# Kernel optimization log

Measured on AMD Instinct MI355X. Metric: run time of the kernel, lower is better.

## Reference

```python
import jax, jax.numpy as jnp
import numpy as np
import math

DIM = 2048
B, Q_LEN, KV_LEN = 8, 128, 4096


def setup_inputs() -> dict:
    key = jax.random.key(0)
    ks = jax.random.split(key, 8)
    x = jax.random.normal(ks[0], (B, Q_LEN, DIM), dtype=jnp.float32)
    mask = jnp.zeros((B, Q_LEN, KV_LEN + Q_LEN), dtype=bool)  # unused by the original forward
    k_cache = jax.random.normal(ks[1], (B, KV_LEN, DIM), dtype=jnp.float32)
    v_cache = jax.random.normal(ks[2], (B, KV_LEN, DIM), dtype=jnp.float32)
    scale = 1.0 / math.sqrt(DIM)
    wq = jax.random.normal(ks[3], (DIM, DIM), dtype=jnp.float32) * scale
    wk = jax.random.normal(ks[4], (DIM, DIM), dtype=jnp.float32) * scale
    wv = jax.random.normal(ks[5], (DIM, DIM), dtype=jnp.float32) * scale
    wo = jax.random.normal(ks[6], (DIM, DIM), dtype=jnp.float32) * scale
    return {"x": x, "mask": mask, "k_cache": k_cache, "v_cache": v_cache,
            "wq": wq, "wk": wk, "wv": wv, "wo": wo}


def reference(x, mask, k_cache, v_cache, wq, wk, wv, wo):
    # Linear layers (torch: y = x @ W^T)
    q = jnp.einsum('bsd,ed->bse', x, wq)
    k_new = jnp.einsum('bsd,ed->bse', x, wk)
    v_new = jnp.einsum('bsd,ed->bse', x, wv)
    # KV-cache growth via concat (the pattern the kernel replaces)
    k = jnp.concatenate([k_cache, k_new], axis=1)  # [B, KV+Q, D]
    v = jnp.concatenate([v_cache, v_new], axis=1)
    scale = 1.0 / math.sqrt(q.shape[-1])
    scores = jnp.einsum('bqd,bkd->bqk', q, k) * scale  # [B, Q, KV+Q]
    attn = jax.nn.softmax(scores, axis=-1)             # NOTE: mask is unused, as in original
    out = jnp.einsum('bqk,bkd->bqd', attn, v)
    return jnp.einsum('bqd,ed->bqe', out, wo)
```

## Files before the change

### kernel.cpp

```cpp
#include <hip/hip_runtime.h>

typedef __bf16 bf16;
typedef __bf16 bf16x4 __attribute__((ext_vector_type(4)));
typedef __bf16 bf16x8 __attribute__((ext_vector_type(8)));
typedef float f32x4 __attribute__((ext_vector_type(4)));

#define DIM   2048
#define BQ    128
#define KVL   4096
#define KVT   4224
#define SCALE 0.022097086912079608f

__device__ __forceinline__ int swz(int row, int col) {
  return row * 64 + (col ^ ((row & 7) << 3));
}

template<int R>
struct PB {
  bf16x8 v[R / 32];
  __device__ __forceinline__ void load(const bf16* __restrict__ src, int ld, int tid) {
    const int r0 = tid >> 3, c = (tid & 7) * 8;
    #pragma unroll
    for (int j = 0; j < R / 32; ++j)
      v[j] = *reinterpret_cast<const bf16x8*>(src + (size_t)(j * 32 + r0) * ld + c);
  }
  __device__ __forceinline__ void write(bf16* dst, int tid) {
    const int r0 = tid >> 3, c = (tid & 7) * 8;
    #pragma unroll
    for (int j = 0; j < R / 32; ++j)
      *reinterpret_cast<bf16x8*>(dst + swz(j * 32 + r0, c)) = v[j];
  }
};

struct PU64 {
  float4 v[4];
  int r0, c;
  __device__ __forceinline__ void init(int tid) { r0 = tid >> 4; c = (tid & 15) * 4; }
  __device__ __forceinline__ void loadF(const float* __restrict__ src, int ld) {
    #pragma unroll
    for (int j = 0; j < 4; ++j)
      v[j] = *reinterpret_cast<const float4*>(src + (size_t)(j * 16 + r0) * ld + c);
  }
  __device__ __forceinline__ void loadB(const bf16* __restrict__ src, int ld) {
    #pragma unroll
    for (int j = 0; j < 4; ++j) {
      bf16x4 t = *reinterpret_cast<const bf16x4*>(src + (size_t)(j * 16 + r0) * ld + c);
      v[j].x = (float)t[0]; v[j].y = (float)t[1]; v[j].z = (float)t[2]; v[j].w = (float)t[3];
    }
  }
  __device__ __forceinline__ void write(bf16* dst) {
    #pragma unroll
    for (int j = 0; j < 4; ++j) {
      bf16x4 b;
      b[0] = (bf16)v[j].x; b[1] = (bf16)v[j].y; b[2] = (bf16)v[j].z; b[3] = (bf16)v[j].w;
      *reinterpret_cast<bf16x4*>(dst + swz(j * 16 + r0, c)) = b;
    }
  }
};

struct PVT {
  float v[16];
  int vn, vk0;
  __device__ __forceinline__ void init(int tid) { vn = tid & 63; vk0 = (tid >> 6) * 16; }
  __device__ __forceinline__ void loadF(const float* __restrict__ src) {
    #pragma unroll
    for (int i = 0; i < 16; ++i) v[i] = src[(size_t)(vk0 + i) * DIM + vn];
  }
  __device__ __forceinline__ void loadB(const bf16* __restrict__ src) {
    #pragma unroll
    for (int i = 0; i < 16; ++i) v[i] = (float)src[(size_t)(vk0 + i) * DIM + vn];
  }
  __device__ __forceinline__ void write(bf16* dst) {
    #pragma unroll
    for (int j = 0; j < 4; ++j) {
      bf16x4 t;
      #pragma unroll
      for (int i = 0; i < 4; ++i) t[i] = (bf16)v[4 * j + i];
      *reinterpret_cast<bf16x4*>(dst + swz(vn, vk0 + 4 * j)) = t;
    }
  }
};

template<int MF, int NF>
__device__ __forceinline__ void mma_tile(const bf16* As, const bf16* Bs,
                                         f32x4 (&acc)[MF][NF], int l, int wm, int wn) {
  const int ar = l & 15;
  const int ak = (l >> 4) * 8;
  bf16x8 a[MF][2], b[NF][2];
  #pragma unroll
  for (int mi = 0; mi < MF; ++mi)
    #pragma unroll
    for (int kk = 0; kk < 2; ++kk)
      a[mi][kk] = *reinterpret_cast<const bf16x8*>(As + swz(wm + mi * 16 + ar, kk * 32 + ak));
  #pragma unroll
  for (int ni = 0; ni < NF; ++ni)
    #pragma unroll
    for (int kk = 0; kk < 2; ++kk)
      b[ni][kk] = *reinterpret_cast<const bf16x8*>(Bs + swz(wn + ni * 16 + ar, kk * 32 + ak));
  #pragma unroll
  for (int kk = 0; kk < 2; ++kk)
    #pragma unroll
    for (int mi = 0; mi < MF; ++mi)
      #pragma unroll
      for (int ni = 0; ni < NF; ++ni)
        acc[mi][ni] = __builtin_amdgcn_mfma_f32_16x16x32_bf16(
            a[mi][kk], b[ni][kk], acc[mi][ni], 0, 0, 0);
}

__global__ __launch_bounds__(256) void k_cvt(const float* __restrict__ x,
    const float* __restrict__ wq, const float* __restrict__ wk,
    const float* __restrict__ wv, const float* __restrict__ wo,
    bf16* __restrict__ xb, bf16* __restrict__ wb) {
  const int seg = blockIdx.y;
  const float* src; bf16* dst; int n; float sc = 1.0f;
  if (seg == 0)      { src = x;  dst = xb;            n = 1024 * DIM; }
  else if (seg == 1) { src = wq; dst = wb;            n = DIM * DIM; sc = SCALE; }
  else if (seg == 2) { src = wk; dst = wb + 1 * DIM * DIM; n = DIM * DIM; }
  else if (seg == 3) { src = wv; dst = wb + 2 * DIM * DIM; n = DIM * DIM; }
  else               { src = wo; dst = wb + 3 * DIM * DIM; n = DIM * DIM; }
  const int i0 = (blockIdx.x * 256 + threadIdx.x) * 8;
  if (i0 >= n) return;
  #pragma unroll
  for (int h = 0; h < 2; ++h) {
    float4 v = *reinterpret_cast<const float4*>(src + i0 + 4 * h);
    bf16x4 b;
    b[0] = (bf16)(v.x * sc); b[1] = (bf16)(v.y * sc);
    b[2] = (bf16)(v.z * sc); b[3] = (bf16)(v.w * sc);
    *reinterpret_cast<bf16x4*>(dst + i0 + 4 * h) = b;
  }
}

__global__ __launch_bounds__(256) void k_qkv(const bf16* __restrict__ xb,
    const bf16* __restrict__ wb,
    bf16* __restrict__ qb, bf16* __restrict__ kb, bf16* __restrict__ vb) {
  __shared__ bf16 As[2][128 * 64];
  __shared__ bf16 Bs[2][64 * 64];
  const int nt = blockIdx.x;
  const int w  = nt >> 5;
  const int col0 = (nt & 31) * 64;
  bf16* __restrict__ O = (w == 0) ? qb : (w == 1) ? kb : vb;
  const int m0 = blockIdx.y * 128;
  const int tid = threadIdx.x, l = tid & 63, wid = tid >> 6;
  const int wm = (wid >> 1) * 64, wn = (wid & 1) * 32;
  const bf16* Ap = xb + (size_t)m0 * DIM;
  const bf16* Bp = wb + (size_t)nt * 64 * DIM;
  PB<128> pa; PB<64> pbb;
  f32x4 acc[4][2] = {};
  pa.load(Ap, DIM, tid); pbb.load(Bp, DIM, tid);
  pa.write(As[0], tid);  pbb.write(Bs[0], tid);
  int cur = 0;
  constexpr int NT = DIM / 64;
  for (int kt = 0; kt < NT; ++kt) {
    if (kt + 1 < NT) { pa.load(Ap + (kt + 1) * 64, DIM, tid); pbb.load(Bp + (kt + 1) * 64, DIM, tid); }
    __syncthreads();
    mma_tile<4, 2>(As[cur], Bs[cur], acc, l, wm, wn);
    if (kt + 1 < NT) { pa.write(As[cur ^ 1], tid); pbb.write(Bs[cur ^ 1], tid); }
    cur ^= 1;
  }
  const int rr = (l >> 4) * 4, cc = l & 15;
  #pragma unroll
  for (int mi = 0; mi < 4; ++mi)
    #pragma unroll
    for (int ni = 0; ni < 2; ++ni)
      #pragma unroll
      for (int r = 0; r < 4; ++r)
        O[(size_t)(m0 + wm + mi * 16 + rr + r) * DIM + col0 + wn + ni * 16 + cc] =
            (bf16)acc[mi][ni][r];
}

__global__ __launch_bounds__(256) void k_scores(const bf16* __restrict__ qb,
    const bf16* __restrict__ kb, const float* __restrict__ kcache,
    float* __restrict__ scores) {
  __shared__ bf16 As[2][128 * 64];
  __shared__ bf16 Bs[2][64 * 64];
  const int nt = blockIdx.x;
  const int b  = blockIdx.y;
  const int tid = threadIdx.x, l = tid & 63, wid = tid >> 6;
  const int wm = (wid >> 1) * 64, wn = (wid & 1) * 32;
  const bf16* Q = qb + (size_t)b * BQ * DIM;
  const bool useCache = (nt < 64);
  const float* Bf = kcache + ((size_t)b * KVL + nt * 64) * DIM;
  const bf16*  Bb = kb + ((size_t)b * BQ + (nt - 64) * 64) * DIM;
  PB<128> pa; PU64 pu; pu.init(tid);
  f32x4 acc[4][2] = {};
  pa.load(Q, DIM, tid);
  if (useCache) pu.loadF(Bf, DIM); else pu.loadB(Bb, DIM);
  pa.write(As[0], tid); pu.write(Bs[0]);
  int cur = 0;
  constexpr int NT = DIM / 64;
  for (int kt = 0; kt < NT; ++kt) {
    if (kt + 1 < NT) {
      pa.load(Q + (kt + 1) * 64, DIM, tid);
      if (useCache) pu.loadF(Bf + (kt + 1) * 64, DIM); else pu.loadB(Bb + (kt + 1) * 64, DIM);
    }
    __syncthreads();
    mma_tile<4, 2>(As[cur], Bs[cur], acc, l, wm, wn);
    if (kt + 1 < NT) { pa.write(As[cur ^ 1], tid); pu.write(Bs[cur ^ 1]); }
    cur ^= 1;
  }
  const int rr = (l >> 4) * 4, cc = l & 15;
  #pragma unroll
  for (int mi = 0; mi < 4; ++mi)
    #pragma unroll
    for (int ni = 0; ni < 2; ++ni)
      #pragma unroll
      for (int r = 0; r < 4; ++r)
        scores[((size_t)b * BQ + wm + mi * 16 + rr + r) * KVT + nt * 64 + wn + ni * 16 + cc] =
            acc[mi][ni][r];
}

__global__ __launch_bounds__(256) void k_softmax(const float* __restrict__ scores,
                                                 bf16* __restrict__ attn) {
  __shared__ float s[KVT];
  __shared__ float red[8];
  const int row = blockIdx.x;
  const int tid = threadIdx.x;
  const size_t base = (size_t)row * KVT;
  float lm = -1e30f;
  for (int i = tid; i < KVT; i += 256) {
    float v = scores[base + i];
    s[i] = v;
    lm = fmaxf(lm, v);
  }
  #pragma unroll
  for (int off = 32; off >= 1; off >>= 1) lm = fmaxf(lm, __shfl_xor(lm, off, 64));
  if ((tid & 63) == 0) red[tid >> 6] = lm;
  __syncthreads();
  const float m = fmaxf(fmaxf(red[0], red[1]), fmaxf(red[2], red[3]));
  float ls = 0.f;
  for (int i = tid; i < KVT; i += 256) {
    float e = __expf(s[i] - m);
    s[i] = e;
    ls += e;
  }
  #pragma unroll
  for (int off = 32; off >= 1; off >>= 1) ls += __shfl_xor(ls, off, 64);
  if ((tid & 63) == 0) red[4 + (tid >> 6)] = ls;
  __syncthreads();
  const float inv = 1.f / (red[4] + red[5] + red[6] + red[7]);
  for (int i = tid; i < KVT; i += 256) attn[base + i] = (bf16)(s[i] * inv);
}

__global__ __launch_bounds__(256) void k_pv(const bf16* __restrict__ attn,
    const float* __restrict__ vcache, const bf16* __restrict__ vb,
    float* __restrict__ pp) {
  __shared__ bf16 As[2][128 * 64];
  __shared__ bf16 VT[2][64 * 64];
  const int n0 = blockIdx.x * 64;
  const int b  = blockIdx.y;
  const int c  = blockIdx.z;
  const int tid = threadIdx.x, l = tid & 63, wid = tid >> 6;
  const int wm = (wid >> 1) * 64, wn = (wid & 1) * 32;
  const bf16* Ap = attn + (size_t)b * BQ * KVT + c * 2112;
  PB<128> pa; PVT pv; pv.init(tid);
  f32x4 acc[4][2] = {};
  auto loadV = [&](int lk) {
    const int grow = c * 2112 + lk * 64;
    if (grow < KVL) pv.loadF(vcache + ((size_t)b * KVL + grow) * DIM + n0);
    else            pv.loadB(vb + ((size_t)b * BQ + (grow - KVL)) * DIM + n0);
  };
  pa.load(Ap, KVT, tid); loadV(0);
  pa.write(As[0], tid);  pv.write(VT[0]);
  int cur = 0;
  constexpr int NT = 33;
  for (int kt = 0; kt < NT; ++kt) {
    if (kt + 1 < NT) { pa.load(Ap + (kt + 1) * 64, KVT, tid); loadV(kt + 1); }
    __syncthreads();
    mma_tile<4, 2>(As[cur], VT[cur], acc, l, wm, wn);
    if (kt + 1 < NT) { pa.write(As[cur ^ 1], tid); pv.write(VT[cur ^ 1]); }
    cur ^= 1;
  }
  float* P = pp + (size_t)c * 1024 * DIM;
  const int rr = (l >> 4) * 4, cc = l & 15;
  #pragma unroll
  for (int mi = 0; mi < 4; ++mi)
    #pragma unroll
    for (int ni = 0; ni < 2; ++ni)
      #pragma unroll
      for (int r = 0; r < 4; ++r)
        P[((size_t)b * BQ + wm + mi * 16 + rr + r) * DIM + n0 + wn + ni * 16 + cc] =
            acc[mi][ni][r];
}

__global__ __launch_bounds__(256) void k_pvcomb(const float* __restrict__ pp,
                                                bf16* __restrict__ ob) {
  const int i0 = (blockIdx.x * 256 + threadIdx.x) * 4;
  float4 a = *reinterpret_cast<const float4*>(pp + i0);
  float4 b = *reinterpret_cast<const float4*>(pp + 1024 * DIM + i0);
  bf16x4 o;
  o[0] = (bf16)(a.x + b.x); o[1] = (bf16)(a.y + b.y);
  o[2] = (bf16)(a.z + b.z); o[3] = (bf16)(a.w + b.w);
  *reinterpret_cast<bf16x4*>(ob + i0) = o;
}

__global__ __launch_bounds__(256) void k_oproj(const bf16* __restrict__ ob,
    const bf16* __restrict__ wob, float* __restrict__ po) {
  __shared__ bf16 As[2][128 * 64];
  __shared__ bf16 Bs[2][64 * 64];
  const int n0 = blockIdx.x * 64;
  const int m0 = blockIdx.y * 128;
  const int kz = blockIdx.z;
  const int tid = threadIdx.x, l = tid & 63, wid = tid >> 6;
  const int wm = (wid >> 1) * 64, wn = (wid & 1) * 32;
  const bf16* Ap = ob  + (size_t)m0 * DIM + kz * 1024;
  const bf16* Bp = wob + (size_t)n0 * DIM + kz * 1024;
  PB<128> pa; PB<64> pbb;
  f32x4 acc[4][2] = {};
  pa.load(Ap, DIM, tid); pbb.load(Bp, DIM, tid);
  pa.write(As[0], tid);  pbb.write(Bs[0], tid);
  int cur = 0;
  constexpr int NT = 16;
  for (int kt = 0; kt < NT; ++kt) {
    if (kt + 1 < NT) { pa.load(Ap + (kt + 1) * 64, DIM, tid); pbb.load(Bp + (kt + 1) * 64, DIM, tid); }
    __syncthreads();
    mma_tile<4, 2>(As[cur], Bs[cur], acc, l, wm, wn);
    if (kt + 1 < NT) { pa.write(As[cur ^ 1], tid); pbb.write(Bs[cur ^ 1], tid); }
    cur ^= 1;
  }
  float* P = po + (size_t)kz * 1024 * DIM;
  const int rr = (l >> 4) * 4, cc = l & 15;
  #pragma unroll
  for (int mi = 0; mi < 4; ++mi)
    #pragma unroll
    for (int ni = 0; ni < 2; ++ni)
      #pragma unroll
      for (int r = 0; r < 4; ++r)
        P[(size_t)(m0 + wm + mi * 16 + rr + r) * DIM + n0 + wn + ni * 16 + cc] =
            acc[mi][ni][r];
}

__global__ __launch_bounds__(256) void k_ocomb(const float* __restrict__ po,
                                               float* __restrict__ out) {
  const int i0 = (blockIdx.x * 256 + threadIdx.x) * 4;
  float4 a = *reinterpret_cast<const float4*>(po + i0);
  float4 b = *reinterpret_cast<const float4*>(po + 1024 * DIM + i0);
  float4 o = {a.x + b.x, a.y + b.y, a.z + b.z, a.w + b.w};
  *reinterpret_cast<float4*>(out + i0) = o;
}

extern "C" void kernel_launch(void* const* d_in, const int* in_sizes, int n_in,
                              void* d_out, int out_size, void* d_ws, size_t ws_size,
                              hipStream_t stream) {
  const float* x      = (const float*)d_in[0];
  const float* kcache = (const float*)d_in[2];
  const float* vcache = (const float*)d_in[3];
  const float* wq     = (const float*)d_in[4];
  const float* wk     = (const float*)d_in[5];
  const float* wv     = (const float*)d_in[6];
  const float* wo     = (const float*)d_in[7];
  float* out = (float*)d_out;

  char* ws = (char*)d_ws;
  bf16*  xb     = (bf16*)(ws + 0);
  bf16*  wb     = (bf16*)(ws + 4194304);
  bf16*  qb     = (bf16*)(ws + 37748736);
  bf16*  kb     = (bf16*)(ws + 41943040);
  bf16*  vb     = (bf16*)(ws + 46137344);
  float* scores = (float*)(ws + 50331648);
  bf16*  attnb  = (bf16*)(ws + 67633152);
  bf16*  obuf   = (bf16*)(ws + 76283904);
  float* pp     = scores;
  bf16*  wob    = wb + (size_t)3 * DIM * DIM;

  k_cvt<<<dim3(2048, 5), 256, 0, stream>>>(x, wq, wk, wv, wo, xb, wb);
  k_qkv<<<dim3(96, 8), 256, 0, stream>>>(xb, wb, qb, kb, vb);
  k_scores<<<dim3(66, 8), 256, 0, stream>>>(qb, kb, kcache, scores);
  k_softmax<<<dim3(1024), 256, 0, stream>>>(scores, attnb);
  k_pv<<<dim3(32, 8, 2), 256, 0, stream>>>(attnb, vcache, vb, pp);
  k_pvcomb<<<dim3(2048), 256, 0, stream>>>(pp, obuf);
  k_oproj<<<dim3(32, 8, 2), 256, 0, stream>>>(obuf, wob, pp);
  k_ocomb<<<dim3(2048), 256, 0, stream>>>(pp, out);
}
```

Before: 245.6 us.

## Stage bf16 tiles via direct global-to-LDS loads and drop o-proj split-K

Replaces the register-staged bf16 tile loads with direct global-to-LDS loads (global_load_lds) using an XOR chunk swizzle in the qkv, scores, pv and oproj GEMMs, and moves the barrier to after the MMA. This is meant to cut VGPR pressure and the extra LDS write instructions, and to let copies overlap compute. The oproj split-K over two halves and its combine kernel are removed so the projection writes the output directly. This saves a launch and a float round trip but halves the oproj grid to 256 blocks. It also depends on the swizzle matching the reader's layout.

```diff
diff --git a/kernel.cpp b/kernel.cpp
--- a/kernel.cpp
+++ b/kernel.cpp
@@ -15,22 +15,24 @@
   return row * 64 + (col ^ ((row & 7) << 3));
 }
 
-template<int R>
-struct PB {
-  bf16x8 v[R / 32];
-  __device__ __forceinline__ void load(const bf16* __restrict__ src, int ld, int tid) {
-    const int r0 = tid >> 3, c = (tid & 7) * 8;
-    #pragma unroll
-    for (int j = 0; j < R / 32; ++j)
-      v[j] = *reinterpret_cast<const bf16x8*>(src + (size_t)(j * 32 + r0) * ld + c);
-  }
-  __device__ __forceinline__ void write(bf16* dst, int tid) {
-    const int r0 = tid >> 3, c = (tid & 7) * 8;
-    #pragma unroll
-    for (int j = 0; j < R / 32; ++j)
-      *reinterpret_cast<bf16x8*>(dst + swz(j * 32 + r0, c)) = v[j];
-  }
-};
+__device__ __forceinline__ void gload16(const bf16* g, bf16* l) {
+  __builtin_amdgcn_global_load_lds(
+      (const __attribute__((address_space(1))) void*)g,
+      (__attribute__((address_space(3))) void*)l, 16, 0, 0);
+}
+
+template<int R, int NW>
+__device__ __forceinline__ void gstage(const bf16* __restrict__ src, int ld,
+                                       bf16* dst, int wid, int lane) {
+  constexpr int OPS = R / (8 * NW);
+  const int rsub = lane >> 3;
+  const int schunk = (lane & 7) ^ (rsub & 7);
+  #pragma unroll
+  for (int j = 0; j < OPS; ++j) {
+    const int row0 = wid * (R / NW) + j * 8;
+    gload16(src + (size_t)(row0 + rsub) * ld + schunk * 8, dst + row0 * 64);
+  }
+}
 
 struct PU64 {
   float4 v[4];
@@ -144,18 +146,18 @@
   const int wm = (wid >> 1) * 64, wn = (wid & 1) * 32;
   const bf16* Ap = xb + (size_t)m0 * DIM;
   const bf16* Bp = wb + (size_t)nt * 64 * DIM;
-  PB<128> pa; PB<64> pbb;
   f32x4 acc[4][2] = {};
-  pa.load(Ap, DIM, tid); pbb.load(Bp, DIM, tid);
-  pa.write(As[0], tid);  pbb.write(Bs[0], tid);
-  int cur = 0;
+  gstage<128, 4>(Ap, DIM, As[0], wid, l);
+  gstage<64, 4>(Bp, DIM, Bs[0], wid, l);
+  __syncthreads();
   constexpr int NT = DIM / 64;
   for (int kt = 0; kt < NT; ++kt) {
-    if (kt + 1 < NT) { pa.load(Ap + (kt + 1) * 64, DIM, tid); pbb.load(Bp + (kt + 1) * 64, DIM, tid); }
+    if (kt + 1 < NT) {
+      gstage<128, 4>(Ap + (kt + 1) * 64, DIM, As[(kt + 1) & 1], wid, l);
+      gstage<64, 4>(Bp + (kt + 1) * 64, DIM, Bs[(kt + 1) & 1], wid, l);
+    }
+    mma_tile<4, 2>(As[kt & 1], Bs[kt & 1], acc, l, wm, wn);
     __syncthreads();
-    mma_tile<4, 2>(As[cur], Bs[cur], acc, l, wm, wn);
-    if (kt + 1 < NT) { pa.write(As[cur ^ 1], tid); pbb.write(Bs[cur ^ 1], tid); }
-    cur ^= 1;
   }
   const int rr = (l >> 4) * 4, cc = l & 15;
   #pragma unroll
@@ -181,22 +183,21 @@
   const bool useCache = (nt < 64);
   const float* Bf = kcache + ((size_t)b * KVL + nt * 64) * DIM;
   const bf16*  Bb = kb + ((size_t)b * BQ + (nt - 64) * 64) * DIM;
-  PB<128> pa; PU64 pu; pu.init(tid);
+  PU64 pu; pu.init(tid);
   f32x4 acc[4][2] = {};
-  pa.load(Q, DIM, tid);
+  gstage<128, 4>(Q, DIM, As[0], wid, l);
   if (useCache) pu.loadF(Bf, DIM); else pu.loadB(Bb, DIM);
-  pa.write(As[0], tid); pu.write(Bs[0]);
-  int cur = 0;
+  pu.write(Bs[0]);
+  __syncthreads();
   constexpr int NT = DIM / 64;
   for (int kt = 0; kt < NT; ++kt) {
     if (kt + 1 < NT) {
-      pa.load(Q + (kt + 1) * 64, DIM, tid);
+      gstage<128, 4>(Q + (kt + 1) * 64, DIM, As[(kt + 1) & 1], wid, l);
       if (useCache) pu.loadF(Bf + (kt + 1) * 64, DIM); else pu.loadB(Bb + (kt + 1) * 64, DIM);
     }
+    mma_tile<4, 2>(As[kt & 1], Bs[kt & 1], acc, l, wm, wn);
+    if (kt + 1 < NT) pu.write(Bs[(kt + 1) & 1]);
     __syncthreads();
-    mma_tile<4, 2>(As[cur], Bs[cur], acc, l, wm, wn);
-    if (kt + 1 < NT) { pa.write(As[cur ^ 1], tid); pu.write(Bs[cur ^ 1]); }
-    cur ^= 1;
   }
   const int rr = (l >> 4) * 4, cc = l & 15;
   #pragma unroll
@@ -252,23 +253,25 @@
   const int tid = threadIdx.x, l = tid & 63, wid = tid >> 6;
   const int wm = (wid >> 1) * 64, wn = (wid & 1) * 32;
   const bf16* Ap = attn + (size_t)b * BQ * KVT + c * 2112;
-  PB<128> pa; PVT pv; pv.init(tid);
+  PVT pv; pv.init(tid);
   f32x4 acc[4][2] = {};
   auto loadV = [&](int lk) {
     const int grow = c * 2112 + lk * 64;
     if (grow < KVL) pv.loadF(vcache + ((size_t)b * KVL + grow) * DIM + n0);
     else            pv.loadB(vb + ((size_t)b * BQ + (grow - KVL)) * DIM + n0);
   };
-  pa.load(Ap, KVT, tid); loadV(0);
-  pa.write(As[0], tid);  pv.write(VT[0]);
-  int cur = 0;
+  gstage<128, 4>(Ap, KVT, As[0], wid, l);
+  loadV(0); pv.write(VT[0]);
+  __syncthreads();
   constexpr int NT = 33;
   for (int kt = 0; kt < NT; ++kt) {
-    if (kt + 1 < NT) { pa.load(Ap + (kt + 1) * 64, KVT, tid); loadV(kt + 1); }
+    if (kt + 1 < NT) {
+      gstage<128, 4>(Ap + (kt + 1) * 64, KVT, As[(kt + 1) & 1], wid, l);
+      loadV(kt + 1);
+    }
+    mma_tile<4, 2>(As[kt & 1], VT[kt & 1], acc, l, wm, wn);
+    if (kt + 1 < NT) pv.write(VT[(kt + 1) & 1]);
     __syncthreads();
-    mma_tile<4, 2>(As[cur], VT[cur], acc, l, wm, wn);
-    if (kt + 1 < NT) { pa.write(As[cur ^ 1], tid); pv.write(VT[cur ^ 1]); }
-    cur ^= 1;
   }
   float* P = pp + (size_t)c * 1024 * DIM;
   const int rr = (l >> 4) * 4, cc = l & 15;
@@ -294,30 +297,28 @@
 }
 
 __global__ __launch_bounds__(256) void k_oproj(const bf16* __restrict__ ob,
-    const bf16* __restrict__ wob, float* __restrict__ po) {
+    const bf16* __restrict__ wob, float* __restrict__ out) {
   __shared__ bf16 As[2][128 * 64];
   __shared__ bf16 Bs[2][64 * 64];
   const int n0 = blockIdx.x * 64;
   const int m0 = blockIdx.y * 128;
-  const int kz = blockIdx.z;
   const int tid = threadIdx.x, l = tid & 63, wid = tid >> 6;
   const int wm = (wid >> 1) * 64, wn = (wid & 1) * 32;
-  const bf16* Ap = ob  + (size_t)m0 * DIM + kz * 1024;
-  const bf16* Bp = wob + (size_t)n0 * DIM + kz * 1024;
-  PB<128> pa; PB<64> pbb;
+  const bf16* Ap = ob  + (size_t)m0 * DIM;
+  const bf16* Bp = wob + (size_t)n0 * DIM;
   f32x4 acc[4][2] = {};
-  pa.load(Ap, DIM, tid); pbb.load(Bp, DIM, tid);
-  pa.write(As[0], tid);  pbb.write(Bs[0], tid);
-  int cur = 0;
-  constexpr int NT = 16;
+  gstage<128, 4>(Ap, DIM, As[0], wid, l);
+  gstage<64, 4>(Bp, DIM, Bs[0], wid, l);
+  __syncthreads();
+  constexpr int NT = DIM / 64;
   for (int kt = 0; kt < NT; ++kt) {
-    if (kt + 1 < NT) { pa.load(Ap + (kt + 1) * 64, DIM, tid); pbb.load(Bp + (kt + 1) * 64, DIM, tid); }
+    if (kt + 1 < NT) {
+      gstage<128, 4>(Ap + (kt + 1) * 64, DIM, As[(kt + 1) & 1], wid, l);
+      gstage<64, 4>(Bp + (kt + 1) * 64, DIM, Bs[(kt + 1) & 1], wid, l);
+    }
+    mma_tile<4, 2>(As[kt & 1], Bs[kt & 1], acc, l, wm, wn);
     __syncthreads();
-    mma_tile<4, 2>(As[cur], Bs[cur], acc, l, wm, wn);
-    if (kt + 1 < NT) { pa.write(As[cur ^ 1], tid); pbb.write(Bs[cur ^ 1], tid); }
-    cur ^= 1;
-  }
-  float* P = po + (size_t)kz * 1024 * DIM;
+  }
   const int rr = (l >> 4) * 4, cc = l & 15;
   #pragma unroll
   for (int mi = 0; mi < 4; ++mi)
@@ -325,17 +326,8 @@
     for (int ni = 0; ni < 2; ++ni)
       #pragma unroll
       for (int r = 0; r < 4; ++r)
-        P[(size_t)(m0 + wm + mi * 16 + rr + r) * DIM + n0 + wn + ni * 16 + cc] =
+        out[(size_t)(m0 + wm + mi * 16 + rr + r) * DIM + n0 + wn + ni * 16 + cc] =
             acc[mi][ni][r];
-}
-
-__global__ __launch_bounds__(256) void k_ocomb(const float* __restrict__ po,
-                                               float* __restrict__ out) {
-  const int i0 = (blockIdx.x * 256 + threadIdx.x) * 4;
-  float4 a = *reinterpret_cast<const float4*>(po + i0);
-  float4 b = *reinterpret_cast<const float4*>(po + 1024 * DIM + i0);
-  float4 o = {a.x + b.x, a.y + b.y, a.z + b.z, a.w + b.w};
-  *reinterpret_cast<float4*>(out + i0) = o;
 }
 
 extern "C" void kernel_launch(void* const* d_in, const int* in_sizes, int n_in,
@@ -359,7 +351,7 @@
   float* scores = (float*)(ws + 50331648);
   bf16*  attnb  = (bf16*)(ws + 67633152);
   bf16*  obuf   = (bf16*)(ws + 76283904);
-  float* pp     = scores;
+  float* pp     = (float*)(ws + 80478208);
   bf16*  wob    = wb + (size_t)3 * DIM * DIM;
 
   k_cvt<<<dim3(2048, 5), 256, 0, stream>>>(x, wq, wk, wv, wo, xb, wb);
@@ -368,6 +360,5 @@
   k_softmax<<<dim3(1024), 256, 0, stream>>>(scores, attnb);
   k_pv<<<dim3(32, 8, 2), 256, 0, stream>>>(attnb, vcache, vb, pp);
   k_pvcomb<<<dim3(2048), 256, 0, stream>>>(pp, obuf);
-  k_oproj<<<dim3(32, 8, 2), 256, 0, stream>>>(obuf, wob, pp);
-  k_ocomb<<<dim3(2048), 256, 0, stream>>>(pp, out);
-}
+  k_oproj<<<dim3(32, 8), 256, 0, stream>>>(obuf, wob, out);
+}
```

Measured after the change: 282.9 us. +15.2%, slower.

## Use 2-wave blocks with larger per-wave tiles and single-buffered LDS in qkv and oproj GEMMs

Applied to the files above, without the earlier changes.

The qkv and output-projection GEMMs now launch 128 threads (2 waves) per 128x64 tile instead of 4. Each wave computes a 64x64 sub-tile (4x4 MFMA fragments), which gives more reuse of each LDS fragment per wave. The LDS double buffer is replaced by a single buffer with two barriers per k-step, with global prefetch into registers still overlapping the MMA. The intent is lower LDS traffic and smaller LDS footprint per block, at the cost of more registers, fewer waves per block to hide latency, and extra sync stalls.

```diff
diff --git a/kernel.cpp b/kernel.cpp
--- a/kernel.cpp
+++ b/kernel.cpp
@@ -15,20 +15,21 @@
   return row * 64 + (col ^ ((row & 7) << 3));
 }
 
-template<int R>
-struct PB {
-  bf16x8 v[R / 32];
+template<int R, int NTHR>
+struct PBg {
+  static constexpr int N8 = R * 64 / (NTHR * 8);
+  bf16x8 v[N8];
   __device__ __forceinline__ void load(const bf16* __restrict__ src, int ld, int tid) {
     const int r0 = tid >> 3, c = (tid & 7) * 8;
     #pragma unroll
-    for (int j = 0; j < R / 32; ++j)
-      v[j] = *reinterpret_cast<const bf16x8*>(src + (size_t)(j * 32 + r0) * ld + c);
+    for (int j = 0; j < N8; ++j)
+      v[j] = *reinterpret_cast<const bf16x8*>(src + (size_t)(j * (NTHR / 8) + r0) * ld + c);
   }
   __device__ __forceinline__ void write(bf16* dst, int tid) {
     const int r0 = tid >> 3, c = (tid & 7) * 8;
     #pragma unroll
-    for (int j = 0; j < R / 32; ++j)
-      *reinterpret_cast<bf16x8*>(dst + swz(j * 32 + r0, c)) = v[j];
+    for (int j = 0; j < N8; ++j)
+      *reinterpret_cast<bf16x8*>(dst + swz(j * (NTHR / 8) + r0, c)) = v[j];
   }
 };
 
@@ -130,41 +131,41 @@
   }
 }
 
-__global__ __launch_bounds__(256) void k_qkv(const bf16* __restrict__ xb,
+__global__ __launch_bounds__(128) void k_qkv(const bf16* __restrict__ xb,
     const bf16* __restrict__ wb,
     bf16* __restrict__ qb, bf16* __restrict__ kb, bf16* __restrict__ vb) {
-  __shared__ bf16 As[2][128 * 64];
-  __shared__ bf16 Bs[2][64 * 64];
+  __shared__ bf16 As[128 * 64];
+  __shared__ bf16 Bs[64 * 64];
   const int nt = blockIdx.x;
   const int w  = nt >> 5;
   const int col0 = (nt & 31) * 64;
   bf16* __restrict__ O = (w == 0) ? qb : (w == 1) ? kb : vb;
   const int m0 = blockIdx.y * 128;
   const int tid = threadIdx.x, l = tid & 63, wid = tid >> 6;
-  const int wm = (wid >> 1) * 64, wn = (wid & 1) * 32;
+  const int wm = wid * 64;
   const bf16* Ap = xb + (size_t)m0 * DIM;
   const bf16* Bp = wb + (size_t)nt * 64 * DIM;
-  PB<128> pa; PB<64> pbb;
-  f32x4 acc[4][2] = {};
-  pa.load(Ap, DIM, tid); pbb.load(Bp, DIM, tid);
-  pa.write(As[0], tid);  pbb.write(Bs[0], tid);
-  int cur = 0;
+  PBg<128, 128> pa; PBg<64, 128> pb;
+  f32x4 acc[4][4] = {};
+  pa.load(Ap, DIM, tid); pb.load(Bp, DIM, tid);
+  pa.write(As, tid);     pb.write(Bs, tid);
+  __syncthreads();
   constexpr int NT = DIM / 64;
   for (int kt = 0; kt < NT; ++kt) {
-    if (kt + 1 < NT) { pa.load(Ap + (kt + 1) * 64, DIM, tid); pbb.load(Bp + (kt + 1) * 64, DIM, tid); }
-    __syncthreads();
-    mma_tile<4, 2>(As[cur], Bs[cur], acc, l, wm, wn);
-    if (kt + 1 < NT) { pa.write(As[cur ^ 1], tid); pbb.write(Bs[cur ^ 1], tid); }
-    cur ^= 1;
+    if (kt + 1 < NT) { pa.load(Ap + (kt + 1) * 64, DIM, tid); pb.load(Bp + (kt + 1) * 64, DIM, tid); }
+    mma_tile<4, 4>(As, Bs, acc, l, wm, 0);
+    __syncthreads();
+    if (kt + 1 < NT) { pa.write(As, tid); pb.write(Bs, tid); }
+    __syncthreads();
   }
   const int rr = (l >> 4) * 4, cc = l & 15;
   #pragma unroll
   for (int mi = 0; mi < 4; ++mi)
     #pragma unroll
-    for (int ni = 0; ni < 2; ++ni)
+    for (int ni = 0; ni < 4; ++ni)
       #pragma unroll
       for (int r = 0; r < 4; ++r)
-        O[(size_t)(m0 + wm + mi * 16 + rr + r) * DIM + col0 + wn + ni * 16 + cc] =
+        O[(size_t)(m0 + wm + mi * 16 + rr + r) * DIM + col0 + ni * 16 + cc] =
             (bf16)acc[mi][ni][r];
 }
 
@@ -181,7 +182,7 @@
   const bool useCache = (nt < 64);
   const float* Bf = kcache + ((size_t)b * KVL + nt * 64) * DIM;
   const bf16*  Bb = kb + ((size_t)b * BQ + (nt - 64) * 64) * DIM;
-  PB<128> pa; PU64 pu; pu.init(tid);
+  PBg<128, 256> pa; PU64 pu; pu.init(tid);
   f32x4 acc[4][2] = {};
   pa.load(Q, DIM, tid);
   if (useCache) pu.loadF(Bf, DIM); else pu.loadB(Bb, DIM);
@@ -252,7 +253,7 @@
   const int tid = threadIdx.x, l = tid & 63, wid = tid >> 6;
   const int wm = (wid >> 1) * 64, wn = (wid & 1) * 32;
   const bf16* Ap = attn + (size_t)b * BQ * KVT + c * 2112;
-  PB<128> pa; PVT pv; pv.init(tid);
+  PBg<128, 256> pa; PVT pv; pv.init(tid);
   f32x4 acc[4][2] = {};
   auto loadV = [&](int lk) {
     const int grow = c * 2112 + lk * 64;
@@ -293,39 +294,39 @@
   *reinterpret_cast<bf16x4*>(ob + i0) = o;
 }
 
-__global__ __launch_bounds__(256) void k_oproj(const bf16* __restrict__ ob,
+__global__ __launch_bounds__(128) void k_oproj(const bf16* __restrict__ ob,
     const bf16* __restrict__ wob, float* __restrict__ po) {
-  __shared__ bf16 As[2][128 * 64];
-  __shared__ bf16 Bs[2][64 * 64];
+  __shared__ bf16 As[128 * 64];
+  __shared__ bf16 Bs[64 * 64];
   const int n0 = blockIdx.x * 64;
   const int m0 = blockIdx.y * 128;
   const int kz = blockIdx.z;
   const int tid = threadIdx.x, l = tid & 63, wid = tid >> 6;
-  const int wm = (wid >> 1) * 64, wn = (wid & 1) * 32;
+  const int wm = wid * 64;
   const bf16* Ap = ob  + (size_t)m0 * DIM + kz * 1024;
   const bf16* Bp = wob + (size_t)n0 * DIM + kz * 1024;
-  PB<128> pa; PB<64> pbb;
-  f32x4 acc[4][2] = {};
-  pa.load(Ap, DIM, tid); pbb.load(Bp, DIM, tid);
-  pa.write(As[0], tid);  pbb.write(Bs[0], tid);
-  int cur = 0;
+  PBg<128, 128> pa; PBg<64, 128> pb;
+  f32x4 acc[4][4] = {};
+  pa.load(Ap, DIM, tid); pb.load(Bp, DIM, tid);
+  pa.write(As, tid);     pb.write(Bs, tid);
+  __syncthreads();
   constexpr int NT = 16;
   for (int kt = 0; kt < NT; ++kt) {
-    if (kt + 1 < NT) { pa.load(Ap + (kt + 1) * 64, DIM, tid); pbb.load(Bp + (kt + 1) * 64, DIM, tid); }
-    __syncthreads();
-    mma_tile<4, 2>(As[cur], Bs[cur], acc, l, wm, wn);
-    if (kt + 1 < NT) { pa.write(As[cur ^ 1], tid); pbb.write(Bs[cur ^ 1], tid); }
-    cur ^= 1;
+    if (kt + 1 < NT) { pa.load(Ap + (kt + 1) * 64, DIM, tid); pb.load(Bp + (kt + 1) * 64, DIM, tid); }
+    mma_tile<4, 4>(As, Bs, acc, l, wm, 0);
+    __syncthreads();
+    if (kt + 1 < NT) { pa.write(As, tid); pb.write(Bs, tid); }
+    __syncthreads();
   }
   float* P = po + (size_t)kz * 1024 * DIM;
   const int rr = (l >> 4) * 4, cc = l & 15;
   #pragma unroll
   for (int mi = 0; mi < 4; ++mi)
     #pragma unroll
-    for (int ni = 0; ni < 2; ++ni)
+    for (int ni = 0; ni < 4; ++ni)
       #pragma unroll
       for (int r = 0; r < 4; ++r)
-        P[(size_t)(m0 + wm + mi * 16 + rr + r) * DIM + n0 + wn + ni * 16 + cc] =
+        P[(size_t)(m0 + wm + mi * 16 + rr + r) * DIM + n0 + ni * 16 + cc] =
             acc[mi][ni][r];
 }
 
@@ -363,11 +364,11 @@
   bf16*  wob    = wb + (size_t)3 * DIM * DIM;
 
   k_cvt<<<dim3(2048, 5), 256, 0, stream>>>(x, wq, wk, wv, wo, xb, wb);
-  k_qkv<<<dim3(96, 8), 256, 0, stream>>>(xb, wb, qb, kb, vb);
+  k_qkv<<<dim3(96, 8), 128, 0, stream>>>(xb, wb, qb, kb, vb);
   k_scores<<<dim3(66, 8), 256, 0, stream>>>(qb, kb, kcache, scores);
   k_softmax<<<dim3(1024), 256, 0, stream>>>(scores, attnb);
   k_pv<<<dim3(32, 8, 2), 256, 0, stream>>>(attnb, vcache, vb, pp);
   k_pvcomb<<<dim3(2048), 256, 0, stream>>>(pp, obuf);
-  k_oproj<<<dim3(32, 8, 2), 256, 0, stream>>>(obuf, wob, pp);
+  k_oproj<<<dim3(32, 8, 2), 128, 0, stream>>>(obuf, wob, pp);
   k_ocomb<<<dim3(2048), 256, 0, stream>>>(pp, out);
 }
```

After: 257.5 us. 1.05x slower.

## Fuse softmax normalization into PV load and drop oproj split-K

Applied to the files above, without the earlier changes.

Softmax now only computes per-row max and inverse sum; the PV GEMM reads fp32 scores and applies exp/normalize while staging tiles into shared memory, removing the bf16 attention buffer round trip. The output projection drops its split-K and combine kernel, writing directly to the output. This trades extra fp32 reads and redundant exp work across PV column blocks, plus lower parallelism in the projection, for fewer launches and less intermediate traffic.

```diff
diff --git a/kernel.cpp b/kernel.cpp
--- a/kernel.cpp
+++ b/kernel.cpp
@@ -15,20 +15,55 @@
   return row * 64 + (col ^ ((row & 7) << 3));
 }
 
-template<int R>
-struct PB {
-  bf16x8 v[R / 32];
+template<int R, int NTHR>
+struct PBg {
+  static constexpr int N8 = R * 64 / (NTHR * 8);
+  bf16x8 v[N8];
   __device__ __forceinline__ void load(const bf16* __restrict__ src, int ld, int tid) {
     const int r0 = tid >> 3, c = (tid & 7) * 8;
     #pragma unroll
-    for (int j = 0; j < R / 32; ++j)
-      v[j] = *reinterpret_cast<const bf16x8*>(src + (size_t)(j * 32 + r0) * ld + c);
+    for (int j = 0; j < N8; ++j)
+      v[j] = *reinterpret_cast<const bf16x8*>(src + (size_t)(j * (NTHR / 8) + r0) * ld + c);
   }
   __device__ __forceinline__ void write(bf16* dst, int tid) {
     const int r0 = tid >> 3, c = (tid & 7) * 8;
     #pragma unroll
-    for (int j = 0; j < R / 32; ++j)
-      *reinterpret_cast<bf16x8*>(dst + swz(j * 32 + r0, c)) = v[j];
+    for (int j = 0; j < N8; ++j)
+      *reinterpret_cast<bf16x8*>(dst + swz(j * (NTHR / 8) + r0, c)) = v[j];
+  }
+};
+
+struct PS {
+  float4 v[8];
+  float m[4], inv[4];
+  int r0, c;
+  __device__ __forceinline__ void init(int tid, const float2* __restrict__ minv) {
+    r0 = tid >> 3; c = (tid & 7) * 8;
+    #pragma unroll
+    for (int j = 0; j < 4; ++j) {
+      float2 t = minv[j * 32 + r0];
+      m[j] = t.x; inv[j] = t.y;
+    }
+  }
+  __device__ __forceinline__ void load(const float* __restrict__ src, int ld) {
+    #pragma unroll
+    for (int j = 0; j < 4; ++j) {
+      const float* p = src + (size_t)(j * 32 + r0) * ld + c;
+      v[2 * j]     = *reinterpret_cast<const float4*>(p);
+      v[2 * j + 1] = *reinterpret_cast<const float4*>(p + 4);
+    }
+  }
+  __device__ __forceinline__ void write(bf16* dst) {
+    #pragma unroll
+    for (int j = 0; j < 4; ++j) {
+      bf16x8 o;
+      #pragma unroll
+      for (int i = 0; i < 4; ++i) {
+        o[i]     = (bf16)(__expf(v[2 * j][i]     - m[j]) * inv[j]);
+        o[4 + i] = (bf16)(__expf(v[2 * j + 1][i] - m[j]) * inv[j]);
+      }
+      *reinterpret_cast<bf16x8*>(dst + swz(j * 32 + r0, c)) = o;
+    }
   }
 };
 
@@ -144,17 +179,17 @@
   const int wm = (wid >> 1) * 64, wn = (wid & 1) * 32;
   const bf16* Ap = xb + (size_t)m0 * DIM;
   const bf16* Bp = wb + (size_t)nt * 64 * DIM;
-  PB<128> pa; PB<64> pbb;
+  PBg<128, 256> pa; PBg<64, 256> pb;
   f32x4 acc[4][2] = {};
-  pa.load(Ap, DIM, tid); pbb.load(Bp, DIM, tid);
-  pa.write(As[0], tid);  pbb.write(Bs[0], tid);
+  pa.load(Ap, DIM, tid); pb.load(Bp, DIM, tid);
+  pa.write(As[0], tid);  pb.write(Bs[0], tid);
   int cur = 0;
   constexpr int NT = DIM / 64;
   for (int kt = 0; kt < NT; ++kt) {
-    if (kt + 1 < NT) { pa.load(Ap + (kt + 1) * 64, DIM, tid); pbb.load(Bp + (kt + 1) * 64, DIM, tid); }
+    if (kt + 1 < NT) { pa.load(Ap + (kt + 1) * 64, DIM, tid); pb.load(Bp + (kt + 1) * 64, DIM, tid); }
     __syncthreads();
     mma_tile<4, 2>(As[cur], Bs[cur], acc, l, wm, wn);
-    if (kt + 1 < NT) { pa.write(As[cur ^ 1], tid); pbb.write(Bs[cur ^ 1], tid); }
+    if (kt + 1 < NT) { pa.write(As[cur ^ 1], tid); pb.write(Bs[cur ^ 1], tid); }
     cur ^= 1;
   }
   const int rr = (l >> 4) * 4, cc = l & 15;
@@ -181,7 +216,7 @@
   const bool useCache = (nt < 64);
   const float* Bf = kcache + ((size_t)b * KVL + nt * 64) * DIM;
   const bf16*  Bb = kb + ((size_t)b * BQ + (nt - 64) * 64) * DIM;
-  PB<128> pa; PU64 pu; pu.init(tid);
+  PBg<128, 256> pa; PU64 pu; pu.init(tid);
   f32x4 acc[4][2] = {};
   pa.load(Q, DIM, tid);
   if (useCache) pu.loadF(Bf, DIM); else pu.loadB(Bb, DIM);
@@ -209,8 +244,8 @@
             acc[mi][ni][r];
 }
 
-__global__ __launch_bounds__(256) void k_softmax(const float* __restrict__ scores,
-                                                 bf16* __restrict__ attn) {
+__global__ __launch_bounds__(256) void k_rowstats(const float* __restrict__ scores,
+                                                  float2* __restrict__ minv) {
   __shared__ float s[KVT];
   __shared__ float red[8];
   const int row = blockIdx.x;
@@ -228,20 +263,19 @@
   __syncthreads();
   const float m = fmaxf(fmaxf(red[0], red[1]), fmaxf(red[2], red[3]));
   float ls = 0.f;
-  for (int i = tid; i < KVT; i += 256) {
-    float e = __expf(s[i] - m);
-    s[i] = e;
-    ls += e;
-  }
+  for (int i = tid; i < KVT; i += 256) ls += __expf(s[i] - m);
   #pragma unroll
   for (int off = 32; off >= 1; off >>= 1) ls += __shfl_xor(ls, off, 64);
   if ((tid & 63) == 0) red[4 + (tid >> 6)] = ls;
   __syncthreads();
-  const float inv = 1.f / (red[4] + red[5] + red[6] + red[7]);
-  for (int i = tid; i < KVT; i += 256) attn[base + i] = (bf16)(s[i] * inv);
-}
-
-__global__ __launch_bounds__(256) void k_pv(const bf16* __restrict__ attn,
+  if (tid == 0) {
+    float inv = 1.f / (red[4] + red[5] + red[6] + red[7]);
+    minv[row] = make_float2(m, inv);
+  }
+}
+
+__global__ __launch_bounds__(256) void k_pv(const float* __restrict__ scores,
+    const float2* __restrict__ minv,
     const float* __restrict__ vcache, const bf16* __restrict__ vb,
     float* __restrict__ pp) {
   __shared__ bf16 As[2][128 * 64];
@@ -251,23 +285,24 @@
   const int c  = blockIdx.z;
   const int tid = threadIdx.x, l = tid & 63, wid = tid >> 6;
   const int wm = (wid >> 1) * 64, wn = (wid & 1) * 32;
-  const bf16* Ap = attn + (size_t)b * BQ * KVT + c * 2112;
-  PB<128> pa; PVT pv; pv.init(tid);
+  const float* Sp = scores + (size_t)b * BQ * KVT + c * 2112;
+  PS pa; pa.init(tid, minv + b * BQ);
+  PVT pv; pv.init(tid);
   f32x4 acc[4][2] = {};
   auto loadV = [&](int lk) {
     const int grow = c * 2112 + lk * 64;
     if (grow < KVL) pv.loadF(vcache + ((size_t)b * KVL + grow) * DIM + n0);
     else            pv.loadB(vb + ((size_t)b * BQ + (grow - KVL)) * DIM + n0);
   };
-  pa.load(Ap, KVT, tid); loadV(0);
-  pa.write(As[0], tid);  pv.write(VT[0]);
+  pa.load(Sp, KVT); loadV(0);
+  pa.write(As[0]);  pv.write(VT[0]);
   int cur = 0;
   constexpr int NT = 33;
   for (int kt = 0; kt < NT; ++kt) {
-    if (kt + 1 < NT) { pa.load(Ap + (kt + 1) * 64, KVT, tid); loadV(kt + 1); }
+    if (kt + 1 < NT) { pa.load(Sp + (kt + 1) * 64, KVT); loadV(kt + 1); }
     __syncthreads();
     mma_tile<4, 2>(As[cur], VT[cur], acc, l, wm, wn);
-    if (kt + 1 < NT) { pa.write(As[cur ^ 1], tid); pv.write(VT[cur ^ 1]); }
+    if (kt + 1 < NT) { pa.write(As[cur ^ 1]); pv.write(VT[cur ^ 1]); }
     cur ^= 1;
   }
   float* P = pp + (size_t)c * 1024 * DIM;
@@ -294,30 +329,28 @@
 }
 
 __global__ __launch_bounds__(256) void k_oproj(const bf16* __restrict__ ob,
-    const bf16* __restrict__ wob, float* __restrict__ po) {
+    const bf16* __restrict__ wob, float* __restrict__ out) {
   __shared__ bf16 As[2][128 * 64];
   __shared__ bf16 Bs[2][64 * 64];
   const int n0 = blockIdx.x * 64;
   const int m0 = blockIdx.y * 128;
-  const int kz = blockIdx.z;
   const int tid = threadIdx.x, l = tid & 63, wid = tid >> 6;
   const int wm = (wid >> 1) * 64, wn = (wid & 1) * 32;
-  const bf16* Ap = ob  + (size_t)m0 * DIM + kz * 1024;
-  const bf16* Bp = wob + (size_t)n0 * DIM + kz * 1024;
-  PB<128> pa; PB<64> pbb;
+  const bf16* Ap = ob  + (size_t)m0 * DIM;
+  const bf16* Bp = wob + (size_t)n0 * DIM;
+  PBg<128, 256> pa; PBg<64, 256> pb;
   f32x4 acc[4][2] = {};
-  pa.load(Ap, DIM, tid); pbb.load(Bp, DIM, tid);
-  pa.write(As[0], tid);  pbb.write(Bs[0], tid);
+  pa.load(Ap, DIM, tid); pb.load(Bp, DIM, tid);
+  pa.write(As[0], tid);  pb.write(Bs[0], tid);
   int cur = 0;
-  constexpr int NT = 16;
+  constexpr int NT = DIM / 64;
   for (int kt = 0; kt < NT; ++kt) {
-    if (kt + 1 < NT) { pa.load(Ap + (kt + 1) * 64, DIM, tid); pbb.load(Bp + (kt + 1) * 64, DIM, tid); }
+    if (kt + 1 < NT) { pa.load(Ap + (kt + 1) * 64, DIM, tid); pb.load(Bp + (kt + 1) * 64, DIM, tid); }
     __syncthreads();
     mma_tile<4, 2>(As[cur], Bs[cur], acc, l, wm, wn);
-    if (kt + 1 < NT) { pa.write(As[cur ^ 1], tid); pbb.write(Bs[cur ^ 1], tid); }
+    if (kt + 1 < NT) { pa.write(As[cur ^ 1], tid); pb.write(Bs[cur ^ 1], tid); }
     cur ^= 1;
   }
-  float* P = po + (size_t)kz * 1024 * DIM;
   const int rr = (l >> 4) * 4, cc = l & 15;
   #pragma unroll
   for (int mi = 0; mi < 4; ++mi)
@@ -325,17 +358,8 @@
     for (int ni = 0; ni < 2; ++ni)
       #pragma unroll
       for (int r = 0; r < 4; ++r)
-        P[(size_t)(m0 + wm + mi * 16 + rr + r) * DIM + n0 + wn + ni * 16 + cc] =
+        out[(size_t)(m0 + wm + mi * 16 + rr + r) * DIM + n0 + wn + ni * 16 + cc] =
             acc[mi][ni][r];
-}
-
-__global__ __launch_bounds__(256) void k_ocomb(const float* __restrict__ po,
-                                               float* __restrict__ out) {
-  const int i0 = (blockIdx.x * 256 + threadIdx.x) * 4;
-  float4 a = *reinterpret_cast<const float4*>(po + i0);
-  float4 b = *reinterpret_cast<const float4*>(po + 1024 * DIM + i0);
-  float4 o = {a.x + b.x, a.y + b.y, a.z + b.z, a.w + b.w};
-  *reinterpret_cast<float4*>(out + i0) = o;
 }
 
 extern "C" void kernel_launch(void* const* d_in, const int* in_sizes, int n_in,
@@ -351,23 +375,22 @@
   float* out = (float*)d_out;
 
   char* ws = (char*)d_ws;
-  bf16*  xb     = (bf16*)(ws + 0);
-  bf16*  wb     = (bf16*)(ws + 4194304);
-  bf16*  qb     = (bf16*)(ws + 37748736);
-  bf16*  kb     = (bf16*)(ws + 41943040);
-  bf16*  vb     = (bf16*)(ws + 46137344);
-  float* scores = (float*)(ws + 50331648);
-  bf16*  attnb  = (bf16*)(ws + 67633152);
-  bf16*  obuf   = (bf16*)(ws + 76283904);
-  float* pp     = scores;
-  bf16*  wob    = wb + (size_t)3 * DIM * DIM;
+  bf16*   xb     = (bf16*)(ws + 0);
+  bf16*   wb     = (bf16*)(ws + 4194304);
+  bf16*   qb     = (bf16*)(ws + 37748736);
+  bf16*   kb     = (bf16*)(ws + 41943040);
+  bf16*   vb     = (bf16*)(ws + 46137344);
+  float*  scores = (float*)(ws + 50331648);
+  float2* minv   = (float2*)(ws + 67633152);
+  bf16*   obuf   = (bf16*)(ws + 76283904);
+  float*  pp     = (float*)(ws + 80478208);
+  bf16*   wob    = wb + (size_t)3 * DIM * DIM;
 
   k_cvt<<<dim3(2048, 5), 256, 0, stream>>>(x, wq, wk, wv, wo, xb, wb);
   k_qkv<<<dim3(96, 8), 256, 0, stream>>>(xb, wb, qb, kb, vb);
   k_scores<<<dim3(66, 8), 256, 0, stream>>>(qb, kb, kcache, scores);
-  k_softmax<<<dim3(1024), 256, 0, stream>>>(scores, attnb);
-  k_pv<<<dim3(32, 8, 2), 256, 0, stream>>>(attnb, vcache, vb, pp);
+  k_rowstats<<<dim3(1024), 256, 0, stream>>>(scores, minv);
+  k_pv<<<dim3(32, 8, 2), 256, 0, stream>>>(scores, minv, vcache, vb, pp);
   k_pvcomb<<<dim3(2048), 256, 0, stream>>>(pp, obuf);
-  k_oproj<<<dim3(32, 8, 2), 256, 0, stream>>>(obuf, wob, pp);
-  k_ocomb<<<dim3(2048), 256, 0, stream>>>(pp, out);
-}
+  k_oproj<<<dim3(32, 8), 256, 0, stream>>>(obuf, wob, out);
+}
```

Measured after the change: 265.4 us. 1.08x slower.
